# Performance work log

Measured on AMD Instinct MI355X. Metric: run time of the kernel, lower is better.

The kernel has to match this reference:

```python
import jax, jax.numpy as jnp
import numpy as np

EPS = 1e-5
K = 20

def knn(x, k):
    # x: (B, 3, N) -> idx (B, N, k) of nearest neighbors (negative sq-dist topk)
    inner = -2.0 * jnp.einsum('bcn,bcm->bnm', x, x)
    xx = jnp.sum(x * x, axis=1)  # (B, N)
    pd = -xx[:, :, None] - inner - xx[:, None, :]
    return jax.lax.top_k(pd, k)[1]

def graph_feature(feats, idx):
    # feats: (B, C, N), idx: (B, N, k) -> (B, 2C, N, k)
    ft = jnp.transpose(feats, (0, 2, 1))  # (B, N, C)
    gathered = jax.vmap(lambda f, i: f[i])(ft, idx)  # (B, N, k, C)
    center = ft[:, :, None, :]  # (B, N, 1, C)
    out = jnp.concatenate([gathered - center,
                           jnp.broadcast_to(center, gathered.shape)], axis=3)
    return jnp.transpose(out, (0, 3, 1, 2))  # (B, 2C, N, k)

def bn2d(h, g, b):
    m = jnp.mean(h, axis=(0, 2, 3), keepdims=True)
    v = jnp.var(h, axis=(0, 2, 3), keepdims=True)
    return (h - m) * jax.lax.rsqrt(v + EPS) * g[None, :, None, None] + b[None, :, None, None]

def bn1d(h, g, b):
    m = jnp.mean(h, axis=(0, 2), keepdims=True)
    v = jnp.var(h, axis=(0, 2), keepdims=True)
    return (h - m) * jax.lax.rsqrt(v + EPS) * g[None, :, None] + b[None, :, None]

def edge_block(x, feats, w, g, b):
    idx = knn(x, K)
    ef = graph_feature(feats, idx)                  # (B, 2C, N, k)
    h = jnp.einsum('bcnk,oc->bonk', ef, w)          # 1x1 conv, no bias
    h = jnp.tanh(bn2d(h, g, b))
    return jnp.max(h, axis=-1)                      # (B, O, N)


def setup_inputs() -> dict:
    key = jax.random.key(0)
    ks = jax.random.split(key, 20)
    B, N, FD, EMB = 8, 2048, 3, 1024
    def w_init(k, o, i):
        return jax.random.normal(k, (o, i), dtype=jnp.float32) * (1.0 / np.sqrt(i))
    inp = {
        'x': jax.random.normal(ks[0], (B, N, 3), dtype=jnp.float32),
        'features': jax.random.normal(ks[1], (B, N, FD), dtype=jnp.float32),
        'w1': w_init(ks[2], 64, 2 * FD),
        'g1': jnp.ones((64,), jnp.float32), 'b1': jnp.zeros((64,), jnp.float32),
        'w2': w_init(ks[3], 64, 128),
        'g2': jnp.ones((64,), jnp.float32), 'b2': jnp.zeros((64,), jnp.float32),
        'w3': w_init(ks[4], 128, 128),
        'g3': jnp.ones((128,), jnp.float32), 'b3': jnp.zeros((128,), jnp.float32),
        'w4': w_init(ks[5], 256, 256),
        'g4': jnp.ones((256,), jnp.float32), 'b4': jnp.zeros((256,), jnp.float32),
        'w5': w_init(ks[6], EMB, 512),
        'g5': jnp.ones((EMB,), jnp.float32), 'b5': jnp.zeros((EMB,), jnp.float32),
    }
    return inp


def reference(x, features, w1, g1, b1, w2, g2, b2, w3, g3, b3, w4, g4, b4, w5, g5, b5):
    xt = jnp.transpose(x, (0, 2, 1))          # (B, 3, N)
    ft = jnp.transpose(features, (0, 2, 1))   # (B, FD, N)
    B = xt.shape[0]
    f1 = edge_block(xt, ft, w1, g1, b1)       # (B, 64, N)
    f2 = edge_block(xt, f1, w2, g2, b2)       # (B, 64, N)
    f3 = edge_block(xt, f2, w3, g3, b3)       # (B, 128, N)
    f4 = edge_block(xt, f3, w4, g4, b4)       # (B, 256, N)
    cat = jnp.concatenate([f1, f2, f3, f4], axis=1)   # (B, 512, N)
    f5 = jnp.tanh(bn1d(jnp.einsum('bcn,oc->bon', cat, w5), g5, b5))  # (B, EMB, N)
    mx = jnp.max(f5, axis=-1)
    av = jnp.mean(f5, axis=-1)
    return jnp.concatenate([mx, av], axis=1)  # (B, 2*EMB)
```

## Files before the change

### kernel.cpp

```cpp
#include <hip/hip_runtime.h>
#include <cstdio>
#include <cstdint>

#define NPTS 2048
#define NB   8
#define KK   20

typedef __attribute__((ext_vector_type(8))) short  short8;
typedef __attribute__((ext_vector_type(8))) unsigned short ushort8;
typedef __attribute__((ext_vector_type(4))) float  f32x4;
typedef unsigned short ushort;
typedef unsigned int   uint;

#define AS1 __attribute__((address_space(1)))
#define AS3 __attribute__((address_space(3)))

__device__ __forceinline__ ushort f2bf(float f) {
    uint u = __float_as_uint(f);
    u += 0x7fffu + ((u >> 16) & 1u);
    return (ushort)(u >> 16);
}
__device__ __forceinline__ float bf2f(ushort s) { return __uint_as_float((uint)s << 16); }

__device__ __forceinline__ void gload16(const ushort* g, ushort* l) {
    __builtin_amdgcn_global_load_lds((const AS1 uint*)(const void*)g,
                                     (AS3 uint*)(void*)l, 16, 0, 0);
}

__global__ __launch_bounds__(512) void knn_kernel(const float* __restrict__ x,
                                                  int* __restrict__ idx)
{
    __shared__ float4 sp[NPTS];
    const int tid = threadIdx.x;
    const int wv = tid >> 6, lane = tid & 63;
    const int gn0 = blockIdx.x * 8;
    const int b = gn0 >> 11;
    const float* xb = x + (size_t)b * NPTS * 3;

    for (int p = tid; p < NPTS; p += 512) {
        const float a0 = xb[p * 3 + 0], a1 = xb[p * 3 + 1], a2 = xb[p * 3 + 2];
        sp[p] = make_float4(a0, a1, a2, a0 * a0 + a1 * a1 + a2 * a2);
    }
    __syncthreads();

    const int n = (gn0 & (NPTS - 1)) + wv;
    const float4 pn = sp[n];
    const float xxn = pn.w;

    float d[32];
#pragma unroll
    for (int i = 0; i < 32; ++i) {
        const float4 pm = sp[lane + i * 64];
        const float dot = pm.x * pn.x + pm.y * pn.y + pm.z * pn.z;
        const float inner = -2.0f * dot;
        d[i] = (-xxn - inner) - pm.w;
    }

    float gv[4]; int gs[4];
#pragma unroll
    for (int g = 0; g < 4; ++g) {
        float v = d[g * 8]; int s = 0;
#pragma unroll
        for (int j = 1; j < 8; ++j)
            if (d[g * 8 + j] > v) { v = d[g * 8 + j]; s = j; }
        gv[g] = v; gs[g] = s;
    }

    int* op = idx + ((size_t)b * NPTS + n) * KK;
    for (int it = 0; it < KK; ++it) {
        float bv = gv[0]; int bm8 = gs[0];
#pragma unroll
        for (int g = 1; g < 4; ++g)
            if (gv[g] > bv) { bv = gv[g]; bm8 = g * 8 + gs[g]; }
        const int m = lane + (bm8 << 6);

        const uint u = __float_as_uint(bv);
        const uint r = (u & 0x80000000u) ? ~u : (u | 0x80000000u);
        unsigned long long key =
            ((unsigned long long)r << 11) | (unsigned)(2047 - m);

#pragma unroll
        for (int s2 = 32; s2; s2 >>= 1) {
            const unsigned long long ok =
                (unsigned long long)__shfl_xor((long long)key, s2);
            key = (ok > key) ? ok : key;
        }
        const int mw = 2047 - (int)(key & 2047u);
        if (lane == 0) op[it] = mw;

        const int mws   = __builtin_amdgcn_readfirstlane(mw);
        const int wslot = mws >> 6;
        const int wgrp  = wslot >> 3;
        const int wj    = wslot & 7;
        const bool iswin = (lane == (mws & 63));

#pragma unroll
        for (int G = 0; G < 4; ++G) {
            if (wgrp == G) {
#pragma unroll
                for (int j = 0; j < 8; ++j)
                    if (j == wj) d[G * 8 + j] = iswin ? -1e38f : d[G * 8 + j];
                float v = d[G * 8]; int s = 0;
#pragma unroll
                for (int j = 1; j < 8; ++j)
                    if (d[G * 8 + j] > v) { v = d[G * 8 + j]; s = j; }
                gv[G] = v; gs[G] = s;
            }
        }
    }
}

__global__ __launch_bounds__(256) void y1_kernel(const float* __restrict__ feats,
                                                 const float* __restrict__ w1,
                                                 float* __restrict__ Y)
{
    __shared__ float w[384];
    const int tid = threadIdx.x;
    for (int i = tid; i < 384; i += 256) w[i] = w1[i];
    __syncthreads();

    const int b  = blockIdx.y;
    const int p  = blockIdx.x * 2 + (tid >> 7);
    const int o2 = tid & 127;
    const int o = o2 & 63, half = o2 >> 6;
    const float* fp = feats + ((size_t)b * NPTS + p) * 3;
    const float f0 = fp[0], f1 = fp[1], f2 = fp[2];
    const float* wr = &w[o * 6 + half * 3];
    Y[((size_t)b * NPTS + p) * 128 + o2] = wr[0] * f0 + wr[1] * f1 + wr[2] * f2;
}

__global__ __launch_bounds__(256) void wsplit_kernel(const float* __restrict__ w2,
                                                     const float* __restrict__ w3,
                                                     const float* __restrict__ w4,
                                                     ushort* q2h, ushort* q2l,
                                                     ushort* q3h, ushort* q3l,
                                                     ushort* q4h, ushort* q4l)
{
    const int t = blockIdx.x * 256 + threadIdx.x;
    float v; ushort *dh, *dl; int off;
    if (t < 8192)        { int i = t;         int m = i >> 6, c = i & 63;  int o = m & 63,  hf = m >> 6; v = w2[o * 128 + hf * 64  + c]; dh = q2h; dl = q2l; off = i; }
    else if (t < 24576)  { int i = t - 8192;  int m = i >> 6, c = i & 63;  int o = m & 127, hf = m >> 7; v = w3[o * 128 + hf * 64  + c]; dh = q3h; dl = q3l; off = i; }
    else if (t < 90112)  { int i = t - 24576; int m = i >> 7, c = i & 127; int o = m & 255, hf = m >> 8; v = w4[o * 256 + hf * 128 + c]; dh = q4h; dl = q4l; off = i; }
    else return;
    const ushort h = f2bf(v);
    dh[off] = h;
    dl[off] = f2bf(v - bf2f(h));
}

__global__ __launch_bounds__(256) void wsplit5_kernel(const float* __restrict__ w5,
                                                      ushort* q5h, ushort* q5l)
{
    const int t = blockIdx.x * 256 + threadIdx.x;
    if (t >= 1024 * 512) return;
    const float v = w5[t];
    const ushort h = f2bf(v);
    q5h[t] = h;
    q5l[t] = f2bf(v - bf2f(h));
}

template<bool PF32, bool STATS, bool SWZ>
__global__ __launch_bounds__(256) void gemm_mfma(const float* __restrict__ Pf,
                                                 const ushort* __restrict__ Ph,
                                                 const ushort* __restrict__ Pl,
                                                 const ushort* __restrict__ Qh,
                                                 const ushort* __restrict__ Ql,
                                                 float* __restrict__ Out,
                                                 double* __restrict__ est,
                                                 int K, int pitchP, int pitchQ, int ldO,
                                                 long strideP, long strideQ, long strideO)
{
    constexpr int PH = 0, PL = 4096, QH = 8192, QL = 12288;
    __shared__ ushort lds_buf[16384];

    const int tid  = threadIdx.x;
    const int wv   = tid >> 6, lane = tid & 63;

    int bx, by, bz;
    if constexpr (SWZ) {
        const int id = blockIdx.x;
        const int J  = (id & 7) * 128 + (id >> 3);
        bx = J & 7; by = (J >> 3) & 15; bz = J >> 7;
    } else { bx = blockIdx.x; by = blockIdx.y; bz = blockIdx.z; }

    const int i0   = bx * 128;
    const int j0   = by * 128;
    const long prow0 = (long)bz * strideP + (long)i0 * pitchP;
    const long qrow0 = (long)bz * strideQ + (long)j0 * pitchQ;

    const int iw = (wv >> 1) * 64;
    const int jw = (wv & 1) * 64;
    const int lr = lane & 15;
    const int lc = lane >> 4;

    f32x4 acc[4][4];
#pragma unroll
    for (int f = 0; f < 4; ++f)
#pragma unroll
        for (int g = 0; g < 4; ++g) acc[f][g] = (f32x4){0.f, 0.f, 0.f, 0.f};

    for (int k0 = 0; k0 < K; k0 += 32) {
        __syncthreads();
        {
            const int r16 = lane >> 2;
            const int cp  = lane & 3;
#pragma unroll
            for (int q = 0; q < 2; ++q) {
                const int row = wv * 32 + q * 16 + r16;
                const int cl  = cp ^ (row & 3);
                const long go = (long)row * pitchQ + k0 + cl * 8;
                gload16(Qh + qrow0 + go, &lds_buf[QH + (wv * 32 + q * 16) * 32]);
                gload16(Ql + qrow0 + go, &lds_buf[QL + (wv * 32 + q * 16) * 32]);
            }
        }
        if constexpr (!PF32) {
            const int r16 = lane >> 2;
            const int cp  = lane & 3;
#pragma unroll
            for (int q = 0; q < 2; ++q) {
                const int row = wv * 32 + q * 16 + r16;
                const int cl  = cp ^ (row & 3);
                const long go = (long)row * pitchP + k0 + cl * 8;
                gload16(Ph + prow0 + go, &lds_buf[PH + (wv * 32 + q * 16) * 32]);
                gload16(Pl + prow0 + go, &lds_buf[PL + (wv * 32 + q * 16) * 32]);
            }
        } else {
#pragma unroll
            for (int r = 0; r < 2; ++r) {
                const int id  = r * 256 + tid;
                const int row = id >> 2, cl = id & 3;
                const int cp  = cl ^ (row & 3);
                const float* gp = Pf + prow0 + (long)row * pitchP + k0 + cl * 8;
                const float4 v0 = *(const float4*)gp;
                const float4 v1 = *(const float4*)(gp + 4);
                const float vv[8] = {v0.x, v0.y, v0.z, v0.w, v1.x, v1.y, v1.z, v1.w};
                ushort8 hi, lo;
#pragma unroll
                for (int e2 = 0; e2 < 8; ++e2) {
                    const ushort h = f2bf(vv[e2]);
                    hi[e2] = h;
                    lo[e2] = f2bf(vv[e2] - bf2f(h));
                }
                *(ushort8*)&lds_buf[PH + row * 32 + cp * 8] = hi;
                *(ushort8*)&lds_buf[PL + row * 32 + cp * 8] = lo;
            }
        }
        asm volatile("s_waitcnt vmcnt(0)" ::: "memory");
        __syncthreads();

        {
            const int cpa = lc ^ (lr & 3);
            short8 ah[4], al[4], bh[4], bl[4];
#pragma unroll
            for (int f = 0; f < 4; ++f) {
                const int ra = (iw + f * 16 + lr) * 32 + cpa * 8;
                ah[f] = *(const short8*)&lds_buf[PH + ra];
                al[f] = *(const short8*)&lds_buf[PL + ra];
                const int rb = (jw + f * 16 + lr) * 32 + cpa * 8;
                bh[f] = *(const short8*)&lds_buf[QH + rb];
                bl[f] = *(const short8*)&lds_buf[QL + rb];
            }
#pragma unroll
            for (int f = 0; f < 4; ++f)
#pragma unroll
                for (int g = 0; g < 4; ++g) {
                    acc[f][g] = __builtin_amdgcn_mfma_f32_16x16x32_bf16(ah[f], bh[g], acc[f][g], 0, 0, 0);
                    acc[f][g] = __builtin_amdgcn_mfma_f32_16x16x32_bf16(ah[f], bl[g], acc[f][g], 0, 0, 0);
                    acc[f][g] = __builtin_amdgcn_mfma_f32_16x16x32_bf16(al[f], bh[g], acc[f][g], 0, 0, 0);
                }
        }
    }

    const long ob = (long)bz * strideO;
#pragma unroll
    for (int f = 0; f < 4; ++f) {
        const int i = i0 + iw + f * 16 + lc * 4;
#pragma unroll
        for (int g = 0; g < 4; ++g) {
            const int j = j0 + jw + g * 16 + lr;
#pragma unroll
            for (int r = 0; r < 4; ++r)
                Out[ob + (long)(i + r) * ldO + j] = acc[f][g][r];
        }
    }

    if constexpr (STATS) {
        const int slab = blockIdx.x & 7;
#pragma unroll
        for (int f = 0; f < 4; ++f)
#pragma unroll
            for (int r = 0; r < 4; ++r) {
                float s = 0.f, s2 = 0.f;
#pragma unroll
                for (int g = 0; g < 4; ++g) {
                    const float v = acc[f][g][r];
                    s += v;
                    s2 = fmaf(v, v, s2);
                }
#pragma unroll
                for (int d2 = 1; d2 <= 8; d2 <<= 1) {
                    s  += __shfl_xor(s, d2);
                    s2 += __shfl_xor(s2, d2);
                }
                if (lr == 0) {
                    const int i = i0 + iw + f * 16 + lc * 4 + r;
                    atomicAdd(&est[(size_t)slab * 2048 + i],        (double)s);
                    atomicAdd(&est[(size_t)slab * 2048 + 1024 + i], (double)s2);
                }
            }
    }
}

template<int O, int NCH>
__global__ __launch_bounds__(256) void edge_apply(const float* __restrict__ Y,
                                                  const int* __restrict__ knn_idx,
                                                  float* __restrict__ mx_out,
                                                  double* __restrict__ st)
{
    constexpr int M = 2 * O;
    constexpr int NPB = 256 / O;
    const int blk = blockIdx.x;
    const int b     = blk & 7;
    const int chunk = blk >> 3;
    const int tid = threadIdx.x;
    const int o   = tid & (O - 1);
    const int sub = tid / O;
    const int n0  = chunk * (NPB * NCH);
    const size_t rowb = (size_t)b * NPTS;
    float s = 0.f, s2 = 0.f;

#pragma unroll
    for (int it = 0; it < NCH; ++it) {
        const int n = n0 + it * NPB + sub;
        const float* yr = Y + (rowb + n) * M;
        const float base = yr[O + o] - yr[o];
        const int* ip = knn_idx + (rowb + n) * KK;
        int mm[KK];
#pragma unroll
        for (int j = 0; j < KK; ++j) mm[j] = ip[j];
        float h[KK];
#pragma unroll
        for (int j = 0; j < KK; ++j) h[j] = Y[(rowb + mm[j]) * M + o];
        float mx = -1e38f;
#pragma unroll
        for (int j = 0; j < KK; ++j) {
            const float v = h[j] + base;
            mx = fmaxf(mx, v);
            s += v;
            s2 = fmaf(v, v, s2);
        }
        mx_out[(rowb + n) * O + o] = mx;
    }
    double* stp = st + (size_t)(chunk & 7) * (2 * O);
    atomicAdd(&stp[o],     (double)s);
    atomicAdd(&stp[O + o], (double)s2);
}

template<int O>
__global__ __launch_bounds__(256) void edge_finalize(const float* __restrict__ mx_in,
                                                     const double* __restrict__ st,
                                                     const float* __restrict__ gamma,
                                                     const float* __restrict__ beta,
                                                     ushort* __restrict__ ch,
                                                     ushort* __restrict__ cl_,
                                                     int c0)
{
    __shared__ float ssc[256], ssh[256];
    const int b = blockIdx.y;
    const int tid = threadIdx.x;
    if (tid < O) {
        double ssum = 0.0, s2sum = 0.0;
#pragma unroll
        for (int sl = 0; sl < 8; ++sl) {
            ssum  += st[(size_t)sl * (2 * O) + tid];
            s2sum += st[(size_t)sl * (2 * O) + O + tid];
        }
        const double cnt = (double)NB * NPTS * KK;
        const double mean = ssum / cnt;
        const double var  = s2sum / cnt - mean * mean;
        const float rs = rsqrtf((float)var + 1e-5f);
        const float sc = gamma[tid] * rs;
        ssc[tid] = sc;
        ssh[tid] = beta[tid] - (float)mean * sc;
    }
    __syncthreads();

    const int o   = tid & (O - 1);
    const int sub = tid / O;
    const int n0  = blockIdx.x * 8;
    constexpr int NPB = 256 / O;
#pragma unroll
    for (int it = 0; it < 8 / NPB; ++it) {
        const int n = n0 + it * NPB + sub;
        const float v = mx_in[((size_t)b * NPTS + n) * O + o];
        const float f = tanhf(fmaf(v, ssc[o], ssh[o]));
        const ushort h = f2bf(f);
        const size_t co = ((size_t)b * NPTS + n) * 512 + c0 + o;
        ch[co]  = h;
        cl_[co] = f2bf(f - bf2f(h));
    }
}

__global__ __launch_bounds__(256) void final_kernel(const float* __restrict__ e,
                                                    const double* __restrict__ st,
                                                    const float* __restrict__ g5,
                                                    const float* __restrict__ b5,
                                                    float* __restrict__ out)
{
    const int b = blockIdx.y;
    const int wv = threadIdx.x >> 6, lane = threadIdx.x & 63;
    const int o = blockIdx.x * 4 + wv;
    double ssum = 0.0, s2sum = 0.0;
#pragma unroll
    for (int sl = 0; sl < 8; ++sl) {
        ssum  += st[(size_t)sl * 2048 + o];
        s2sum += st[(size_t)sl * 2048 + 1024 + o];
    }
    const double cnt = (double)NB * NPTS;
    const double mean = ssum / cnt;
    const double var  = s2sum / cnt - mean * mean;
    const float rs = rsqrtf((float)var + 1e-5f);
    const float sc = g5[o] * rs;
    const float sh = b5[o] - (float)mean * sc;
    const float* row = e + ((size_t)(b * 1024 + o)) * NPTS;
    float mx = -1e38f, sm = 0.f;
    for (int n = lane; n < NPTS; n += 64) {
        const float v = tanhf(fmaf(row[n], sc, sh));
        mx = fmaxf(mx, v);
        sm += v;
    }
#pragma unroll
    for (int d = 32; d > 0; d >>= 1) {
        mx = fmaxf(mx, __shfl_xor(mx, d));
        sm += __shfl_xor(sm, d);
    }
    if (lane == 0) {
        out[(size_t)b * 2048 + o]        = mx;
        out[(size_t)b * 2048 + 1024 + o] = sm * (1.0f / 2048.0f);
    }
}

extern "C" void kernel_launch(void* const* d_in, const int* in_sizes, int n_in,
                              void* d_out, int out_size, void* d_ws, size_t ws_size,
                              hipStream_t stream)
{
    (void)in_sizes; (void)n_in; (void)out_size;
    const float* x  = (const float*)d_in[0];
    const float* ft = (const float*)d_in[1];
    const float* w1 = (const float*)d_in[2];
    const float* g1 = (const float*)d_in[3];
    const float* b1 = (const float*)d_in[4];
    const float* w2 = (const float*)d_in[5];
    const float* g2 = (const float*)d_in[6];
    const float* b2 = (const float*)d_in[7];
    const float* w3 = (const float*)d_in[8];
    const float* g3 = (const float*)d_in[9];
    const float* b3 = (const float*)d_in[10];
    const float* w4 = (const float*)d_in[11];
    const float* g4 = (const float*)d_in[12];
    const float* b4 = (const float*)d_in[13];
    const float* w5 = (const float*)d_in[14];
    const float* g5 = (const float*)d_in[15];
    const float* b5 = (const float*)d_in[16];
    float* out = (float*)d_out;

    const size_t STATS_OFF = 0;
    const size_t ESTAT_OFF = 131072;
    const size_t IDX_OFF   = 262144;
    const size_t Q2H_OFF   = 1572864,  Q2L_OFF = 1589248;
    const size_t Q3H_OFF   = 1605632,  Q3L_OFF = 1638400;
    const size_t Q4H_OFF   = 1671168,  Q4L_OFF = 1802240;
    const size_t CTH_OFF   = 1933312;
    const size_t CTL_OFF   = 18710528;
    const size_t Y_OFF     = 35487744;
    const size_t MX_OFF    = 69042176;
    const size_t NEED_BASE = 102596608;
    const size_t Q5H_OFF   = 102596608, Q5L_OFF = 103645184;
    const size_t NEED_FULL = 104693760;
    if (ws_size < NEED_BASE) {
        fprintf(stderr, "kernel_launch: ws too small (%zu < %zu)\n", ws_size, NEED_BASE);
        return;
    }
    const bool presplit = (ws_size >= NEED_FULL);

    char* ws = (char*)d_ws;
    double* stats  = (double*)(ws + STATS_OFF);
    double* estats = (double*)(ws + ESTAT_OFF);
    int*    idx    = (int*)(ws + IDX_OFF);
    ushort* q2h = (ushort*)(ws + Q2H_OFF); ushort* q2l = (ushort*)(ws + Q2L_OFF);
    ushort* q3h = (ushort*)(ws + Q3H_OFF); ushort* q3l = (ushort*)(ws + Q3L_OFF);
    ushort* q4h = (ushort*)(ws + Q4H_OFF); ushort* q4l = (ushort*)(ws + Q4L_OFF);
    ushort* q5h = (ushort*)(ws + Q5H_OFF); ushort* q5l = (ushort*)(ws + Q5L_OFF);
    ushort* cth = (ushort*)(ws + CTH_OFF); ushort* ctl = (ushort*)(ws + CTL_OFF);
    float*  Y   = (float*)(ws + Y_OFF);
    float*  mxb = (float*)(ws + MX_OFF);
    float*  e   = (float*)(ws + Y_OFF);

    hipMemsetAsync(ws, 0, 262144, stream);

    knn_kernel<<<NB * NPTS / 8, 512, 0, stream>>>(x, idx);
    wsplit_kernel<<<352, 256, 0, stream>>>(w2, w3, w4, q2h, q2l, q3h, q3l, q4h, q4l);
    if (presplit)
        wsplit5_kernel<<<2048, 256, 0, stream>>>(w5, q5h, q5l);

    y1_kernel<<<dim3(NPTS / 2, NB), 256, 0, stream>>>(ft, w1, Y);
    edge_apply<64, 2><<<2048, 256, 0, stream>>>(Y, idx, mxb, stats + 0 * 4096);
    edge_finalize<64><<<dim3(256, NB), 256, 0, stream>>>(mxb, stats + 0 * 4096, g1, b1, cth, ctl, 0);

    gemm_mfma<false, false, false><<<dim3(16, 1, 8), 256, 0, stream>>>(
        nullptr, cth + 0, ctl + 0, q2h, q2l, Y, nullptr,
        64, 512, 64, 128, (long)NPTS * 512, 0, (long)NPTS * 128);
    edge_apply<64, 2><<<2048, 256, 0, stream>>>(Y, idx, mxb, stats + 1 * 4096);
    edge_finalize<64><<<dim3(256, NB), 256, 0, stream>>>(mxb, stats + 1 * 4096, g2, b2, cth, ctl, 64);

    gemm_mfma<false, false, false><<<dim3(16, 2, 8), 256, 0, stream>>>(
        nullptr, cth + 64, ctl + 64, q3h, q3l, Y, nullptr,
        64, 512, 64, 256, (long)NPTS * 512, 0, (long)NPTS * 256);
    edge_apply<128, 4><<<2048, 256, 0, stream>>>(Y, idx, mxb, stats + 2 * 4096);
    edge_finalize<128><<<dim3(256, NB), 256, 0, stream>>>(mxb, stats + 2 * 4096, g3, b3, cth, ctl, 128);

    gemm_mfma<false, false, false><<<dim3(16, 4, 8), 256, 0, stream>>>(
        nullptr, cth + 128, ctl + 128, q4h, q4l, Y, nullptr,
        128, 512, 128, 512, (long)NPTS * 512, 0, (long)NPTS * 512);
    edge_apply<256, 8><<<2048, 256, 0, stream>>>(Y, idx, mxb, stats + 3 * 4096);
    edge_finalize<256><<<dim3(256, NB), 256, 0, stream>>>(mxb, stats + 3 * 4096, g4, b4, cth, ctl, 256);

    if (presplit) {
        gemm_mfma<false, true, true><<<1024, 256, 0, stream>>>(
            nullptr, q5h, q5l, cth, ctl, e, estats,
            512, 512, 512, 2048, 0, (long)NPTS * 512, (long)1024 * 2048);
    } else {
        gemm_mfma<true, true, true><<<1024, 256, 0, stream>>>(
            w5, nullptr, nullptr, cth, ctl, e, estats,
            512, 512, 512, 2048, 0, (long)NPTS * 512, (long)1024 * 2048);
    }
    final_kernel<<<dim3(256, NB), 256, 0, stream>>>(e, estats, g5, b5, out);
}
```

Measured before the change: 392.3 us.

## Double-buffer LDS tiles in split-bf16 MFMA GEMM to overlap loads with compute

Doubles the shared-memory buffer and restructures the K loop so the next tile's global-to-LDS loads are issued before the MFMAs on the current tile, with partial vmcnt waits and raw barriers. It also changes the XOR swizzle from row&3 to (row>>1)&3 to reduce LDS bank conflicts. The intent is to hide global load latency behind matrix math. The cost is twice the LDS per block, which can lower occupancy, plus hand-tuned waitcnt logic that depends on the exact load count.

```diff
diff --git a/kernel.cpp b/kernel.cpp
--- a/kernel.cpp
+++ b/kernel.cpp
@@ -170,7 +170,8 @@
                                                  long strideP, long strideQ, long strideO)
 {
     constexpr int PH = 0, PL = 4096, QH = 8192, QL = 12288;
-    __shared__ ushort lds_buf[16384];
+    constexpr int BUF = 16384;
+    __shared__ ushort lds_buf[32768];
 
     const int tid  = threadIdx.x;
     const int wv   = tid >> 6, lane = tid & 63;
@@ -198,37 +199,32 @@
 #pragma unroll
         for (int g = 0; g < 4; ++g) acc[f][g] = (f32x4){0.f, 0.f, 0.f, 0.f};
 
-    for (int k0 = 0; k0 < K; k0 += 32) {
-        __syncthreads();
-        {
-            const int r16 = lane >> 2;
-            const int cp  = lane & 3;
+    auto STAGE = [&](int k0, int bb) {
+        const int r16 = lane >> 2;
+        const int cp  = lane & 3;
+#pragma unroll
+        for (int q = 0; q < 2; ++q) {
+            const int row = wv * 32 + q * 16 + r16;
+            const int cl  = cp ^ ((row >> 1) & 3);
+            const long go = (long)row * pitchQ + k0 + cl * 8;
+            gload16(Qh + qrow0 + go, &lds_buf[bb + QH + (wv * 32 + q * 16) * 32]);
+            gload16(Ql + qrow0 + go, &lds_buf[bb + QL + (wv * 32 + q * 16) * 32]);
+        }
+        if constexpr (!PF32) {
 #pragma unroll
             for (int q = 0; q < 2; ++q) {
                 const int row = wv * 32 + q * 16 + r16;
-                const int cl  = cp ^ (row & 3);
-                const long go = (long)row * pitchQ + k0 + cl * 8;
-                gload16(Qh + qrow0 + go, &lds_buf[QH + (wv * 32 + q * 16) * 32]);
-                gload16(Ql + qrow0 + go, &lds_buf[QL + (wv * 32 + q * 16) * 32]);
-            }
-        }
-        if constexpr (!PF32) {
-            const int r16 = lane >> 2;
-            const int cp  = lane & 3;
-#pragma unroll
-            for (int q = 0; q < 2; ++q) {
-                const int row = wv * 32 + q * 16 + r16;
-                const int cl  = cp ^ (row & 3);
+                const int cl  = cp ^ ((row >> 1) & 3);
                 const long go = (long)row * pitchP + k0 + cl * 8;
-                gload16(Ph + prow0 + go, &lds_buf[PH + (wv * 32 + q * 16) * 32]);
-                gload16(Pl + prow0 + go, &lds_buf[PL + (wv * 32 + q * 16) * 32]);
+                gload16(Ph + prow0 + go, &lds_buf[bb + PH + (wv * 32 + q * 16) * 32]);
+                gload16(Pl + prow0 + go, &lds_buf[bb + PL + (wv * 32 + q * 16) * 32]);
             }
         } else {
 #pragma unroll
             for (int r = 0; r < 2; ++r) {
-                const int id  = r * 256 + tid;
-                const int row = id >> 2, cl = id & 3;
-                const int cp  = cl ^ (row & 3);
+                const int id2 = r * 256 + tid;
+                const int row = id2 >> 2, cl = id2 & 3;
+                const int cpw = cl ^ ((row >> 1) & 3);
                 const float* gp = Pf + prow0 + (long)row * pitchP + k0 + cl * 8;
                 const float4 v0 = *(const float4*)gp;
                 const float4 v1 = *(const float4*)(gp + 4);
@@ -240,34 +236,52 @@
                     hi[e2] = h;
                     lo[e2] = f2bf(vv[e2] - bf2f(h));
                 }
-                *(ushort8*)&lds_buf[PH + row * 32 + cp * 8] = hi;
-                *(ushort8*)&lds_buf[PL + row * 32 + cp * 8] = lo;
+                *(ushort8*)&lds_buf[bb + PH + row * 32 + cpw * 8] = hi;
+                *(ushort8*)&lds_buf[bb + PL + row * 32 + cpw * 8] = lo;
             }
         }
-        asm volatile("s_waitcnt vmcnt(0)" ::: "memory");
-        __syncthreads();
-
-        {
-            const int cpa = lc ^ (lr & 3);
-            short8 ah[4], al[4], bh[4], bl[4];
-#pragma unroll
-            for (int f = 0; f < 4; ++f) {
-                const int ra = (iw + f * 16 + lr) * 32 + cpa * 8;
-                ah[f] = *(const short8*)&lds_buf[PH + ra];
-                al[f] = *(const short8*)&lds_buf[PL + ra];
-                const int rb = (jw + f * 16 + lr) * 32 + cpa * 8;
-                bh[f] = *(const short8*)&lds_buf[QH + rb];
-                bl[f] = *(const short8*)&lds_buf[QL + rb];
+    };
+
+    const int NT  = K >> 5;
+    const int cpa = lc ^ ((lr >> 1) & 3);
+    int bb = 0;
+
+    STAGE(0, 0);
+
+    for (int t = 0; t < NT; ++t) {
+        if (t + 1 < NT) {
+            STAGE((t + 1) << 5, bb ^ BUF);
+            if constexpr (PF32)
+                asm volatile("s_waitcnt vmcnt(0) lgkmcnt(0)" ::: "memory");
+            else
+                asm volatile("s_waitcnt vmcnt(8)" ::: "memory");
+        } else {
+            asm volatile("s_waitcnt vmcnt(0) lgkmcnt(0)" ::: "memory");
+        }
+        __builtin_amdgcn_s_barrier();
+        __builtin_amdgcn_sched_barrier(0);
+
+        short8 ah[4], al[4], bh[4], bl[4];
+#pragma unroll
+        for (int f = 0; f < 4; ++f) {
+            const int ra = (iw + f * 16 + lr) * 32 + cpa * 8;
+            ah[f] = *(const short8*)&lds_buf[bb + PH + ra];
+            al[f] = *(const short8*)&lds_buf[bb + PL + ra];
+            const int rb = (jw + f * 16 + lr) * 32 + cpa * 8;
+            bh[f] = *(const short8*)&lds_buf[bb + QH + rb];
+            bl[f] = *(const short8*)&lds_buf[bb + QL + rb];
+        }
+#pragma unroll
+        for (int f = 0; f < 4; ++f)
+#pragma unroll
+            for (int g = 0; g < 4; ++g) {
+                acc[f][g] = __builtin_amdgcn_mfma_f32_16x16x32_bf16(ah[f], bh[g], acc[f][g], 0, 0, 0);
+                acc[f][g] = __builtin_amdgcn_mfma_f32_16x16x32_bf16(ah[f], bl[g], acc[f][g], 0, 0, 0);
+                acc[f][g] = __builtin_amdgcn_mfma_f32_16x16x32_bf16(al[f], bh[g], acc[f][g], 0, 0, 0);
             }
-#pragma unroll
-            for (int f = 0; f < 4; ++f)
-#pragma unroll
-                for (int g = 0; g < 4; ++g) {
-                    acc[f][g] = __builtin_amdgcn_mfma_f32_16x16x32_bf16(ah[f], bh[g], acc[f][g], 0, 0, 0);
-                    acc[f][g] = __builtin_amdgcn_mfma_f32_16x16x32_bf16(ah[f], bl[g], acc[f][g], 0, 0, 0);
-                    acc[f][g] = __builtin_amdgcn_mfma_f32_16x16x32_bf16(al[f], bh[g], acc[f][g], 0, 0, 0);
-                }
-        }
+
+        __builtin_amdgcn_s_barrier();
+        bb ^= BUF;
     }
 
     const long ob = (long)bz * strideO;
```

Result: faster. 377.2 us (-3.8%).
